# Performance work log

Hardware: AMD Instinct MI355X
Metric: run time of the kernel (lower is better)

Reference implementation:

```python
import jax, jax.numpy as jnp
import numpy as np
from jax import lax

K = 5  # kernel size
PAD = (K - 1) // 2


def setup_inputs() -> dict:
    key = jax.random.key(0)
    k1, k2, k3 = jax.random.split(key, 3)
    B, C, H, W = 16, 3, 256, 256
    x = jax.random.normal(k1, (B, C, H, W), dtype=jnp.float32)
    # Conv2d(3 -> 25, kernel=5) params, PyTorch-style fan-in init scale
    fan_in = C * K * K
    bound = 1.0 / np.sqrt(fan_in)
    conv_w = jax.random.uniform(k2, (K * K, C, K, K), dtype=jnp.float32, minval=-bound, maxval=bound)
    conv_b = jax.random.uniform(k3, (K * K,), dtype=jnp.float32, minval=-bound, maxval=bound)
    return {"x": x, "conv_w": conv_w, "conv_b": conv_b}


def reference(x, conv_w, conv_b):
    B, C, H, W = x.shape
    # weights = conv(x): [B, 25, H, W], one scalar weight per tap per pixel
    w = lax.conv_general_dilated(
        x, conv_w, window_strides=(1, 1), padding=((PAD, PAD), (PAD, PAD)),
        dimension_numbers=("NCHW", "OIHW", "NCHW"),
    ) + conv_b[None, :, None, None]
    # dynamic per-pixel 5x5 weighted neighborhood aggregation (zero-padded)
    xp = jnp.pad(x, ((0, 0), (0, 0), (PAD, PAD), (PAD, PAD)))
    out = jnp.zeros_like(x)
    k = 0
    for i in range(K):
        for j in range(K):
            # w[:, k] broadcasts over channels; xp slice is the (i,j)-shifted input
            out = out + w[:, k:k + 1] * xp[:, :, i:i + H, j:j + W]
            k += 1
    return out + x  # residual
```

## Files before the change

kernel.cpp:

```cpp
#include <hip/hip_runtime.h>
#include <stdint.h>

typedef __fp16    half2v __attribute__((ext_vector_type(2)));
typedef _Float16  f16x8  __attribute__((ext_vector_type(8)));
typedef float     f32x4  __attribute__((ext_vector_type(4)));
typedef uint32_t  u32x4  __attribute__((ext_vector_type(4)));

#define KSZ    5
#define NBATCH 16
#define NC     3
#define NH     256
#define NW     256
#define TW     16
#define TH     16
#define TROWS  20
#define TWRD   12
#define CPLANE (TROWS * TWRD)
#define COPYW  (NC * CPLANE)
#define PTS    20
#define NUNIT  (COPYW / 2)

__device__ __forceinline__ uint32_t pack_f16x2(float lo, float hi) {
    half2v h = __builtin_amdgcn_cvt_pkrtz(lo, hi);
    return __builtin_bit_cast(uint32_t, h);
}

__device__ __forceinline__ int pair_of(int s, int d) {
    return (d < 2) ? (2 * s + d) : (8 + 2 * s + (d - 2));
}

__global__ void prep_AB(const float* __restrict__ cw, const float* __restrict__ cb,
                        uint32_t* __restrict__ Atab, float* __restrict__ cbv)
{
    int idx = threadIdx.x + blockIdx.x * 256;
    if (idx < 1536) {
        int d  = idx & 3;
        int fl = (idx >> 2) & 15;
        int s  = (idx >> 6) & 3;
        int t3 = idx >> 8;
        int c  = t3 % 3, mt = t3 / 3;
        int vf = mt * 16 + fl;
        int P  = pair_of(s, d);
        float lo = 0.0f, hi = 0.0f;
        if (vf < 30 && (vf % 6) != 5 && P < 15) {
            int f = (vf / 6) * 5 + (vf % 6);
            int i = P / 3, q = P - 3 * i;
            const float* base = cw + f * 75 + c * 25 + i * 5;
            lo = base[2 * q];
            if (q < 2) hi = base[2 * q + 1];
        }
        Atab[idx] = pack_f16x2(lo, hi);
    } else if (idx < 1568) {
        int vf = idx - 1536;
        float v = 0.0f;
        if (vf < 30 && (vf % 6) != 5) v = cb[(vf / 6) * 5 + (vf % 6)];
        cbv[vf] = v;
    }
}

__global__ __launch_bounds__(256, 4)
void highorder24(const float* __restrict__ x,
                 const uint32_t* __restrict__ Atab,
                 const float* __restrict__ cbv,
                 float* __restrict__ out)
{
    __shared__ uint32_t lds_t[2 * COPYW];
    __shared__ uint32_t pbuf[TH * 16 * PTS];

    const int tid = threadIdx.x;
    const int l   = tid & 63;
    const int w   = tid >> 6;
    const int fl  = l & 15;
    const int s   = l >> 4;

    const int bx  = blockIdx.x & 15;
    const int by  = (blockIdx.x >> 4) & 15;
    const int b   = blockIdx.x >> 8;
    const int bw0 = bx * TW;
    const int bh0 = by * TH;

    const float* xb = x + (size_t)b * NC * NH * NW;

    u32x4 afr[6];
    const u32x4* At4 = (const u32x4*)Atab;
    #pragma unroll
    for (int t3 = 0; t3 < 6; ++t3)
        afr[t3] = At4[(t3 * 4 + s) * 16 + fl];
    const f32x4* cbv4 = (const f32x4*)cbv;
    const f32x4 cbA = cbv4[s];
    const f32x4 cbB = cbv4[4 + s];

    #pragma unroll
    for (int it = 0; it < 2; ++it) {
        int u = tid + it * 256;
        if (u < NUNIT) {
            int c   = u / 120;
            int rem = u - c * 120;
            int r   = rem / 6;
            int j   = rem - r * 6;
            int gh  = bh0 + r - 2;
            int g0  = bw0 + 4 * j - 2;
            bool rowok = (unsigned)gh < NH;
            const float* row = xb + c * NH * NW + gh * NW;
            float x0, x1, x2, x3, x4;
            if (rowok && g0 >= 0 && g0 + 4 < NW) {
                f32x4 v = *reinterpret_cast<const f32x4*>(row + g0);
                x0 = v[0]; x1 = v[1]; x2 = v[2]; x3 = v[3];
                x4 = row[g0 + 4];
            } else {
                x0 = (rowok && (unsigned)(g0)     < NW) ? row[g0]     : 0.0f;
                x1 = (rowok && (unsigned)(g0 + 1) < NW) ? row[g0 + 1] : 0.0f;
                x2 = (rowok && (unsigned)(g0 + 2) < NW) ? row[g0 + 2] : 0.0f;
                x3 = (rowok && (unsigned)(g0 + 3) < NW) ? row[g0 + 3] : 0.0f;
                x4 = (rowok && (unsigned)(g0 + 4) < NW) ? row[g0 + 4] : 0.0f;
            }
            const int idx0 = 2 * u;
            uint2 wa; wa.x = pack_f16x2(x0, x1); wa.y = pack_f16x2(x2, x3);
            uint2 wb; wb.x = pack_f16x2(x1, x2); wb.y = pack_f16x2(x3, x4);
            *reinterpret_cast<uint2*>(&lds_t[idx0])         = wa;
            *reinterpret_cast<uint2*>(&lds_t[COPYW + idx0]) = wb;
        }
    }
    __syncthreads();

    int woff[4];
    #pragma unroll
    for (int d = 0; d < 4; ++d) {
        int P = pair_of(s, d);
        int i = P / 3, q = P - 3 * i;
        woff[d] = (P == 15) ? 0 : (i * TWRD + q);
    }
    const int abase = ((fl & 1) ? COPYW : 0) + (fl >> 1);

    #pragma unroll
    for (int g = 0; g < 4; ++g) {
        const int py = w * 4 + g;
        const int bg = abase + py * TWRD;

        u32x4 bv[3];
        #pragma unroll
        for (int c = 0; c < 3; ++c)
            #pragma unroll
            for (int d = 0; d < 4; ++d)
                bv[c][d] = lds_t[bg + c * CPLANE + woff[d]];

        f32x4 a0 = cbA, a1 = cbB;
        #pragma unroll
        for (int c = 0; c < 3; ++c) {
            f16x8 B = __builtin_bit_cast(f16x8, bv[c]);
            a0 = __builtin_amdgcn_mfma_f32_16x16x32_f16(
                     __builtin_bit_cast(f16x8, afr[c]),     B, a0, 0, 0, 0);
            a1 = __builtin_amdgcn_mfma_f32_16x16x32_f16(
                     __builtin_bit_cast(f16x8, afr[3 + c]), B, a1, 0, 0, 0);
        }

        uint32_t wq0 = pack_f16x2(a0[0], a0[1]);
        uint32_t wq1 = pack_f16x2(a0[2], a0[3]);
        uint32_t wq2 = pack_f16x2(a1[0], a1[1]);
        uint32_t wq3 = pack_f16x2(a1[2], a1[3]);

        const int pb = (py * 16 + fl) * PTS;
        uint2 w01; w01.x = wq0; w01.y = wq1;
        uint2 w23; w23.x = wq2; w23.y = wq3;
        *reinterpret_cast<uint2*>(&pbuf[pb + 2 * s])     = w01;
        *reinterpret_cast<uint2*>(&pbuf[pb + 8 + 2 * s]) = w23;
    }

    const int px  = tid & 15;
    const int py2 = tid >> 4;
    const uint32_t* basep = lds_t + ((px & 1) ? COPYW : 0) + (px >> 1);

    uint32_t nb[45];
    #pragma unroll
    for (int c = 0; c < NC; ++c)
        #pragma unroll
        for (int i = 0; i < KSZ; ++i)
            #pragma unroll
            for (int q = 0; q < 3; ++q)
                nb[c * 15 + i * 3 + q] =
                    basep[c * CPLANE + (py2 + i) * TWRD + q];

    __syncthreads();

    u32x4 wp4[4];
    const int rb = (py2 * 16 + px) * PTS;
    #pragma unroll
    for (int r = 0; r < 4; ++r)
        wp4[r] = *reinterpret_cast<const u32x4*>(&pbuf[rb + 4 * r]);

    float* ob = out + (size_t)b * NC * NH * NW
                    + (size_t)(bh0 + py2) * NW + (bw0 + px);
    #pragma unroll
    for (int c = 0; c < NC; ++c) {
        uint32_t accA = nb[c * 15 + 7] & 0xFFFFu;
        uint32_t accB = 0u;
        #pragma unroll
        for (int t = 0; t < 8; ++t)
            asm("v_pk_fma_f16 %0, %1, %2, %0"
                : "+v"(accA)
                : "v"(wp4[t >> 2][t & 3]), "v"(nb[c * 15 + t]));
        #pragma unroll
        for (int t = 8; t < 15; ++t)
            asm("v_pk_fma_f16 %0, %1, %2, %0"
                : "+v"(accB)
                : "v"(wp4[t >> 2][t & 3]), "v"(nb[c * 15 + t]));
        half2v hA = __builtin_bit_cast(half2v, accA);
        half2v hB = __builtin_bit_cast(half2v, accB);
        ob[(size_t)c * NH * NW] =
            ((float)hA.x + (float)hA.y) + ((float)hB.x + (float)hB.y);
    }
}

extern "C" void kernel_launch(void* const* d_in, const int* in_sizes, int n_in,
                              void* d_out, int out_size, void* d_ws, size_t ws_size,
                              hipStream_t stream)
{
    const float* x  = (const float*)d_in[0];
    const float* cw = (const float*)d_in[1];
    const float* cb = (const float*)d_in[2];
    float* out      = (float*)d_out;
    uint32_t* Atab  = (uint32_t*)d_ws;
    float*    cbv   = (float*)((char*)d_ws + 6144);

    prep_AB<<<7, 256, 0, stream>>>(cw, cb, Atab, cbv);

    dim3 grid(NBATCH * (NH / TH) * (NW / TW));
    highorder24<<<grid, 256, 0, stream>>>(x, Atab, cbv, out);
}
```

Baseline: 27.79 us.

## Process two batch images per block with loads for both issued up front

Each block now handles the same spatial tile for two batch images. Both images' input tiles are loaded into two separate LDS buffers in one pass, which raises memory-level parallelism, and the compute stages then run back to back for each image. The grid is halved and launch bounds raised to 5 blocks per SM. In exchange, LDS per block grows, an extra barrier is added, and register pressure may rise.

```diff
diff --git a/kernel.cpp b/kernel.cpp
--- a/kernel.cpp
+++ b/kernel.cpp
@@ -58,13 +58,14 @@
     }
 }
 
-__global__ __launch_bounds__(256, 4)
-void highorder24(const float* __restrict__ x,
+__global__ __launch_bounds__(256, 5)
+void highorder25(const float* __restrict__ x,
                  const uint32_t* __restrict__ Atab,
                  const float* __restrict__ cbv,
                  float* __restrict__ out)
 {
-    __shared__ uint32_t lds_t[2 * COPYW];
+    __shared__ uint32_t ldsA[2 * COPYW];
+    __shared__ uint32_t ldsB[2 * COPYW];
     __shared__ uint32_t pbuf[TH * 16 * PTS];
 
     const int tid = threadIdx.x;
@@ -75,11 +76,14 @@
 
     const int bx  = blockIdx.x & 15;
     const int by  = (blockIdx.x >> 4) & 15;
-    const int b   = blockIdx.x >> 8;
+    const int bp  = blockIdx.x >> 8;
+    const int b0  = bp * 2;
     const int bw0 = bx * TW;
     const int bh0 = by * TH;
-
-    const float* xb = x + (size_t)b * NC * NH * NW;
+    const size_t bstride = (size_t)NC * NH * NW;
+
+    const float* xb0 = x + (size_t)b0 * bstride;
+    const float* xb1 = xb0 + bstride;
 
     u32x4 afr[6];
     const u32x4* At4 = (const u32x4*)Atab;
@@ -101,24 +105,38 @@
             int gh  = bh0 + r - 2;
             int g0  = bw0 + 4 * j - 2;
             bool rowok = (unsigned)gh < NH;
-            const float* row = xb + c * NH * NW + gh * NW;
-            float x0, x1, x2, x3, x4;
+            const int roff = c * NH * NW + (rowok ? gh : 0) * NW;
+            const float* rowp0 = xb0 + roff;
+            const float* rowp1 = xb1 + roff;
+            float x0, x1, x2, x3, x4, y0, y1, y2, y3, y4;
             if (rowok && g0 >= 0 && g0 + 4 < NW) {
-                f32x4 v = *reinterpret_cast<const f32x4*>(row + g0);
-                x0 = v[0]; x1 = v[1]; x2 = v[2]; x3 = v[3];
-                x4 = row[g0 + 4];
+                f32x4 v0 = *reinterpret_cast<const f32x4*>(rowp0 + g0);
+                f32x4 v1 = *reinterpret_cast<const f32x4*>(rowp1 + g0);
+                x0 = v0[0]; x1 = v0[1]; x2 = v0[2]; x3 = v0[3];
+                x4 = rowp0[g0 + 4];
+                y0 = v1[0]; y1 = v1[1]; y2 = v1[2]; y3 = v1[3];
+                y4 = rowp1[g0 + 4];
             } else {
-                x0 = (rowok && (unsigned)(g0)     < NW) ? row[g0]     : 0.0f;
-                x1 = (rowok && (unsigned)(g0 + 1) < NW) ? row[g0 + 1] : 0.0f;
-                x2 = (rowok && (unsigned)(g0 + 2) < NW) ? row[g0 + 2] : 0.0f;
-                x3 = (rowok && (unsigned)(g0 + 3) < NW) ? row[g0 + 3] : 0.0f;
-                x4 = (rowok && (unsigned)(g0 + 4) < NW) ? row[g0 + 4] : 0.0f;
+                bool k0 = rowok && (unsigned)(g0)     < NW;
+                bool k1 = rowok && (unsigned)(g0 + 1) < NW;
+                bool k2 = rowok && (unsigned)(g0 + 2) < NW;
+                bool k3 = rowok && (unsigned)(g0 + 3) < NW;
+                bool k4 = rowok && (unsigned)(g0 + 4) < NW;
+                x0 = k0 ? rowp0[g0]     : 0.0f;  y0 = k0 ? rowp1[g0]     : 0.0f;
+                x1 = k1 ? rowp0[g0 + 1] : 0.0f;  y1 = k1 ? rowp1[g0 + 1] : 0.0f;
+                x2 = k2 ? rowp0[g0 + 2] : 0.0f;  y2 = k2 ? rowp1[g0 + 2] : 0.0f;
+                x3 = k3 ? rowp0[g0 + 3] : 0.0f;  y3 = k3 ? rowp1[g0 + 3] : 0.0f;
+                x4 = k4 ? rowp0[g0 + 4] : 0.0f;  y4 = k4 ? rowp1[g0 + 4] : 0.0f;
             }
             const int idx0 = 2 * u;
             uint2 wa; wa.x = pack_f16x2(x0, x1); wa.y = pack_f16x2(x2, x3);
             uint2 wb; wb.x = pack_f16x2(x1, x2); wb.y = pack_f16x2(x3, x4);
-            *reinterpret_cast<uint2*>(&lds_t[idx0])         = wa;
-            *reinterpret_cast<uint2*>(&lds_t[COPYW + idx0]) = wb;
+            *reinterpret_cast<uint2*>(&ldsA[idx0])         = wa;
+            *reinterpret_cast<uint2*>(&ldsA[COPYW + idx0]) = wb;
+            uint2 wc; wc.x = pack_f16x2(y0, y1); wc.y = pack_f16x2(y2, y3);
+            uint2 wd; wd.x = pack_f16x2(y1, y2); wd.y = pack_f16x2(y3, y4);
+            *reinterpret_cast<uint2*>(&ldsB[idx0])         = wc;
+            *reinterpret_cast<uint2*>(&ldsB[COPYW + idx0]) = wd;
         }
     }
     __syncthreads();
@@ -131,6 +149,9 @@
         woff[d] = (P == 15) ? 0 : (i * TWRD + q);
     }
     const int abase = ((fl & 1) ? COPYW : 0) + (fl >> 1);
+    const int px  = tid & 15;
+    const int py2 = tid >> 4;
+    const int rb  = (py2 * 16 + px) * PTS;
 
     #pragma unroll
     for (int g = 0; g < 4; ++g) {
@@ -142,7 +163,7 @@
         for (int c = 0; c < 3; ++c)
             #pragma unroll
             for (int d = 0; d < 4; ++d)
-                bv[c][d] = lds_t[bg + c * CPLANE + woff[d]];
+                bv[c][d] = ldsA[bg + c * CPLANE + woff[d]];
 
         f32x4 a0 = cbA, a1 = cbB;
         #pragma unroll
@@ -166,48 +187,123 @@
         *reinterpret_cast<uint2*>(&pbuf[pb + 8 + 2 * s]) = w23;
     }
 
-    const int px  = tid & 15;
-    const int py2 = tid >> 4;
-    const uint32_t* basep = lds_t + ((px & 1) ? COPYW : 0) + (px >> 1);
-
     uint32_t nb[45];
-    #pragma unroll
-    for (int c = 0; c < NC; ++c)
-        #pragma unroll
-        for (int i = 0; i < KSZ; ++i)
-            #pragma unroll
-            for (int q = 0; q < 3; ++q)
-                nb[c * 15 + i * 3 + q] =
-                    basep[c * CPLANE + (py2 + i) * TWRD + q];
-
+    {
+        const uint32_t* basep = ldsA + ((px & 1) ? COPYW : 0) + (px >> 1);
+        #pragma unroll
+        for (int c = 0; c < NC; ++c)
+            #pragma unroll
+            for (int i = 0; i < KSZ; ++i)
+                #pragma unroll
+                for (int q = 0; q < 3; ++q)
+                    nb[c * 15 + i * 3 + q] =
+                        basep[c * CPLANE + (py2 + i) * TWRD + q];
+    }
     __syncthreads();
 
     u32x4 wp4[4];
-    const int rb = (py2 * 16 + px) * PTS;
     #pragma unroll
     for (int r = 0; r < 4; ++r)
         wp4[r] = *reinterpret_cast<const u32x4*>(&pbuf[rb + 4 * r]);
-
-    float* ob = out + (size_t)b * NC * NH * NW
-                    + (size_t)(bh0 + py2) * NW + (bw0 + px);
-    #pragma unroll
-    for (int c = 0; c < NC; ++c) {
-        uint32_t accA = nb[c * 15 + 7] & 0xFFFFu;
-        uint32_t accB = 0u;
-        #pragma unroll
-        for (int t = 0; t < 8; ++t)
-            asm("v_pk_fma_f16 %0, %1, %2, %0"
-                : "+v"(accA)
-                : "v"(wp4[t >> 2][t & 3]), "v"(nb[c * 15 + t]));
-        #pragma unroll
-        for (int t = 8; t < 15; ++t)
-            asm("v_pk_fma_f16 %0, %1, %2, %0"
-                : "+v"(accB)
-                : "v"(wp4[t >> 2][t & 3]), "v"(nb[c * 15 + t]));
-        half2v hA = __builtin_bit_cast(half2v, accA);
-        half2v hB = __builtin_bit_cast(half2v, accB);
-        ob[(size_t)c * NH * NW] =
-            ((float)hA.x + (float)hA.y) + ((float)hB.x + (float)hB.y);
+    __syncthreads();
+
+    {
+        float* ob = out + (size_t)b0 * bstride
+                        + (size_t)(bh0 + py2) * NW + (bw0 + px);
+        #pragma unroll
+        for (int c = 0; c < NC; ++c) {
+            uint32_t accA = nb[c * 15 + 7] & 0xFFFFu;
+            uint32_t accB = 0u;
+            #pragma unroll
+            for (int t = 0; t < 8; ++t)
+                asm("v_pk_fma_f16 %0, %1, %2, %0"
+                    : "+v"(accA)
+                    : "v"(wp4[t >> 2][t & 3]), "v"(nb[c * 15 + t]));
+            #pragma unroll
+            for (int t = 8; t < 15; ++t)
+                asm("v_pk_fma_f16 %0, %1, %2, %0"
+                    : "+v"(accB)
+                    : "v"(wp4[t >> 2][t & 3]), "v"(nb[c * 15 + t]));
+            half2v hA = __builtin_bit_cast(half2v, accA);
+            half2v hB = __builtin_bit_cast(half2v, accB);
+            ob[(size_t)c * NH * NW] =
+                ((float)hA.x + (float)hA.y) + ((float)hB.x + (float)hB.y);
+        }
+    }
+
+    #pragma unroll
+    for (int g = 0; g < 4; ++g) {
+        const int py = w * 4 + g;
+        const int bg = abase + py * TWRD;
+
+        u32x4 bv[3];
+        #pragma unroll
+        for (int c = 0; c < 3; ++c)
+            #pragma unroll
+            for (int d = 0; d < 4; ++d)
+                bv[c][d] = ldsB[bg + c * CPLANE + woff[d]];
+
+        f32x4 a0 = cbA, a1 = cbB;
+        #pragma unroll
+        for (int c = 0; c < 3; ++c) {
+            f16x8 B = __builtin_bit_cast(f16x8, bv[c]);
+            a0 = __builtin_amdgcn_mfma_f32_16x16x32_f16(
+                     __builtin_bit_cast(f16x8, afr[c]),     B, a0, 0, 0, 0);
+            a1 = __builtin_amdgcn_mfma_f32_16x16x32_f16(
+                     __builtin_bit_cast(f16x8, afr[3 + c]), B, a1, 0, 0, 0);
+        }
+
+        uint32_t wq0 = pack_f16x2(a0[0], a0[1]);
+        uint32_t wq1 = pack_f16x2(a0[2], a0[3]);
+        uint32_t wq2 = pack_f16x2(a1[0], a1[1]);
+        uint32_t wq3 = pack_f16x2(a1[2], a1[3]);
+
+        const int pb = (py * 16 + fl) * PTS;
+        uint2 w01; w01.x = wq0; w01.y = wq1;
+        uint2 w23; w23.x = wq2; w23.y = wq3;
+        *reinterpret_cast<uint2*>(&pbuf[pb + 2 * s])     = w01;
+        *reinterpret_cast<uint2*>(&pbuf[pb + 8 + 2 * s]) = w23;
+    }
+
+    {
+        const uint32_t* basep = ldsB + ((px & 1) ? COPYW : 0) + (px >> 1);
+        #pragma unroll
+        for (int c = 0; c < NC; ++c)
+            #pragma unroll
+            for (int i = 0; i < KSZ; ++i)
+                #pragma unroll
+                for (int q = 0; q < 3; ++q)
+                    nb[c * 15 + i * 3 + q] =
+                        basep[c * CPLANE + (py2 + i) * TWRD + q];
+    }
+    __syncthreads();
+
+    #pragma unroll
+    for (int r = 0; r < 4; ++r)
+        wp4[r] = *reinterpret_cast<const u32x4*>(&pbuf[rb + 4 * r]);
+
+    {
+        float* ob = out + (size_t)(b0 + 1) * bstride
+                        + (size_t)(bh0 + py2) * NW + (bw0 + px);
+        #pragma unroll
+        for (int c = 0; c < NC; ++c) {
+            uint32_t accA = nb[c * 15 + 7] & 0xFFFFu;
+            uint32_t accB = 0u;
+            #pragma unroll
+            for (int t = 0; t < 8; ++t)
+                asm("v_pk_fma_f16 %0, %1, %2, %0"
+                    : "+v"(accA)
+                    : "v"(wp4[t >> 2][t & 3]), "v"(nb[c * 15 + t]));
+            #pragma unroll
+            for (int t = 8; t < 15; ++t)
+                asm("v_pk_fma_f16 %0, %1, %2, %0"
+                    : "+v"(accB)
+                    : "v"(wp4[t >> 2][t & 3]), "v"(nb[c * 15 + t]));
+            half2v hA = __builtin_bit_cast(half2v, accA);
+            half2v hB = __builtin_bit_cast(half2v, accB);
+            ob[(size_t)c * NH * NW] =
+                ((float)hA.x + (float)hA.y) + ((float)hB.x + (float)hB.y);
+        }
     }
 }
 
@@ -224,6 +320,6 @@
 
     prep_AB<<<7, 256, 0, stream>>>(cw, cb, Atab, cbv);
 
-    dim3 grid(NBATCH * (NH / TH) * (NW / TW));
-    highorder24<<<grid, 256, 0, stream>>>(x, Atab, cbv, out);
-}
+    dim3 grid((NH / TH) * (NW / TW) * (NBATCH / 2));
+    highorder25<<<grid, 256, 0, stream>>>(x, Atab, cbv, out);
+}
```

Measured after the change: 32.21 us. 15.9% more time.
